# Kernel optimization log

Hardware: AMD Instinct MI355X
Metric: run time of the kernel (lower is better)

The kernel has to match this reference:

```python
import jax, jax.numpy as jnp
import numpy as np

B, IN_DIM, HID, OUT_DIM, K = 16384, 400, 24, 4096, 64


def setup_inputs() -> dict:
    key = jax.random.key(0)
    ks = jax.random.split(key, 20)
    bnd = 1.0 / np.sqrt(IN_DIM)

    def factorized_eps(k, shape):
        # sign(x)*sqrt(|x|) of small gaussian noise, outer-product factorized
        if len(shape) == 2:
            ko, ki = jax.random.split(k)
            eo = jax.random.normal(ko, (shape[0],)) * 0.001
            ei = jax.random.normal(ki, (shape[1],)) * 0.001
            f = lambda v: jnp.sign(v) * jnp.sqrt(jnp.abs(v))
            return jnp.outer(f(eo), f(ei))
        e = jax.random.normal(k, shape) * 0.001
        return jnp.sign(e) * jnp.sqrt(jnp.abs(e))

    sig2 = 0.5 / np.sqrt(HID)
    sig3 = 0.5 / np.sqrt(OUT_DIM)
    bnd24 = 1.0 / np.sqrt(HID)
    return {
        "x": jax.random.normal(ks[0], (B, IN_DIM), dtype=jnp.float32),
        "possible_moves": jax.random.randint(ks[1], (B, K), 0, OUT_DIM),
        "W1": jax.random.uniform(ks[2], (HID, IN_DIM), minval=-bnd, maxval=bnd),
        "b1": jax.random.uniform(ks[3], (HID,), minval=-bnd, maxval=bnd),
        "mu_w2": jax.random.uniform(ks[4], (HID, HID), minval=-bnd24, maxval=bnd24),
        "mu_b2": jax.random.uniform(ks[5], (HID,), minval=-bnd24, maxval=bnd24),
        "sigma_w2": jnp.full((HID, HID), sig2, dtype=jnp.float32),
        "sigma_b2": jnp.full((HID,), sig2, dtype=jnp.float32),
        "eps_w2": factorized_eps(ks[6], (HID, HID)),
        "eps_b2": factorized_eps(ks[7], (HID,)),
        "mu_w3": jax.random.uniform(ks[8], (OUT_DIM, HID), minval=-bnd24, maxval=bnd24),
        "mu_b3": jax.random.uniform(ks[9], (OUT_DIM,), minval=-bnd24, maxval=bnd24),
        "sigma_w3": jnp.full((OUT_DIM, HID), sig3, dtype=jnp.float32),
        "sigma_b3": jnp.full((OUT_DIM,), sig3, dtype=jnp.float32),
        "eps_w3": factorized_eps(ks[10], (OUT_DIM, HID)),
        "eps_b3": factorized_eps(ks[11], (OUT_DIM,)),
    }


def reference(x, possible_moves, W1, b1, mu_w2, mu_b2, sigma_w2, sigma_b2,
              eps_w2, eps_b2, mu_w3, mu_b3, sigma_w3, sigma_b3, eps_w3, eps_b3):
    h = jax.nn.relu(x @ W1.T + b1)
    w2 = mu_w2 + sigma_w2 * eps_w2
    h = jax.nn.relu(h @ w2.T + (mu_b2 + sigma_b2 * eps_b2))
    w3 = mu_w3 + sigma_w3 * eps_w3
    logits = h @ w3.T + (mu_b3 + sigma_b3 * eps_b3)  # [B, OUT_DIM]
    # scatter 1.0 at legal-move indices per row (vectorized LegalSoftmax)
    rows = jnp.arange(logits.shape[0])[:, None]
    mask = jnp.zeros(logits.shape, logits.dtype).at[rows, possible_moves].set(1.0)
    filtered = logits * mask
    return jnp.where(filtered == 0, -jnp.inf, filtered)
```

## Files before the change

### kernel.cpp

```cpp
#include <hip/hip_runtime.h>
#include <math.h>

#define BATCH 16384
#define IN_DIM 400
#define HID 24
#define OUT_DIM 4096
#define KMOV 64

#define SENT_BITS 0xFF7F0000u

__global__ __launch_bounds__(256) void precompute_w3(
    const float* __restrict__ mu_w3, const float* __restrict__ sigma_w3,
    const float* __restrict__ eps_w3, const float* __restrict__ mu_b3,
    const float* __restrict__ sigma_b3, const float* __restrict__ eps_b3,
    float* __restrict__ w3eff, float* __restrict__ b3eff) {
    const int stride = gridDim.x * blockDim.x;
    for (int i = blockIdx.x * blockDim.x + threadIdx.x; i < OUT_DIM * HID; i += stride)
        w3eff[i] = mu_w3[i] + sigma_w3[i] * eps_w3[i];
    for (int i = blockIdx.x * blockDim.x + threadIdx.x; i < OUT_DIM; i += stride)
        b3eff[i] = mu_b3[i] + sigma_b3[i] * eps_b3[i];
}

template <bool PRE>
__global__ __launch_bounds__(256) void noisy_fused(
    const float* __restrict__ x, const int* __restrict__ moves,
    const float* __restrict__ W1, const float* __restrict__ b1,
    const float* __restrict__ mu_w2, const float* __restrict__ mu_b2,
    const float* __restrict__ sigma_w2, const float* __restrict__ sigma_b2,
    const float* __restrict__ eps_w2, const float* __restrict__ eps_b2,
    const float* __restrict__ mu_w3, const float* __restrict__ mu_b3,
    const float* __restrict__ sigma_w3, const float* __restrict__ sigma_b3,
    const float* __restrict__ eps_w3, const float* __restrict__ eps_b3,
    const float* __restrict__ w3eff, const float* __restrict__ b3eff,
    float* __restrict__ out) {
    __shared__ float xs[IN_DIM];
    __shared__ float w2s[HID * HID];
    __shared__ float b2s[HID];
    __shared__ float h1s[HID];
    __shared__ float h2s[HID];

    const int tid = threadIdx.x;
    const int row = blockIdx.x;

    const float* xrow = x + (size_t)row * IN_DIM;
    for (int i = tid; i < IN_DIM; i += 256) xs[i] = xrow[i];
    for (int i = tid; i < HID * HID; i += 256)
        w2s[i] = mu_w2[i] + sigma_w2[i] * eps_w2[i];
    if (tid < HID) b2s[tid] = mu_b2[tid] + sigma_b2[tid] * eps_b2[tid];
    __syncthreads();

    if (tid < HID * 8) {
        const int u = tid >> 3, s = tid & 7;
        const float* w = W1 + u * IN_DIM + s * 50;
        const float* xp = xs + s * 50;
        float acc = 0.f;
#pragma unroll
        for (int k = 0; k < 50; ++k) acc += xp[k] * w[k];
        acc += __shfl_down(acc, 4, 8);
        acc += __shfl_down(acc, 2, 8);
        acc += __shfl_down(acc, 1, 8);
        if (s == 0) h1s[u] = fmaxf(acc + b1[u], 0.f);
    }
    __syncthreads();

    if (tid < HID) {
        float acc = b2s[tid];
#pragma unroll
        for (int j = 0; j < HID; ++j) acc += h1s[j] * w2s[tid * HID + j];
        h2s[tid] = fmaxf(acc, 0.f);
    }
    __syncthreads();

    const float SENT = __uint_as_float(SENT_BITS);
    float val = SENT;
    int idx = 0;
    if (tid < KMOV) {
        idx = moves[(size_t)row * KMOV + tid];
        float acc;
        if (PRE) {
            acc = b3eff[idx];
            const float4* wr = (const float4*)(w3eff + idx * HID);
#pragma unroll
            for (int q = 0; q < 6; ++q) {
                float4 w4 = wr[q];
                acc += h2s[q * 4 + 0] * w4.x + h2s[q * 4 + 1] * w4.y +
                       h2s[q * 4 + 2] * w4.z + h2s[q * 4 + 3] * w4.w;
            }
        } else {
            acc = mu_b3[idx] + sigma_b3[idx] * eps_b3[idx];
            const float4* mr = (const float4*)(mu_w3 + idx * HID);
            const float4* sr = (const float4*)(sigma_w3 + idx * HID);
            const float4* er = (const float4*)(eps_w3 + idx * HID);
#pragma unroll
            for (int q = 0; q < 6; ++q) {
                float4 m4 = mr[q], s4 = sr[q], e4 = er[q];
                acc += h2s[q * 4 + 0] * (m4.x + s4.x * e4.x) +
                       h2s[q * 4 + 1] * (m4.y + s4.y * e4.y) +
                       h2s[q * 4 + 2] * (m4.z + s4.z * e4.z) +
                       h2s[q * 4 + 3] * (m4.w + s4.w * e4.w);
            }
        }
        if (acc != 0.f) val = acc;
    }

    const float4 n4 = make_float4(SENT, SENT, SENT, SENT);
    float4* orow = (float4*)(out + (size_t)row * OUT_DIM);
#pragma unroll
    for (int i = 0; i < 4; ++i) orow[i * 256 + tid] = n4;
    __syncthreads();

    if (tid < KMOV) out[(size_t)row * OUT_DIM + idx] = val;
}

extern "C" void kernel_launch(void* const* d_in, const int* in_sizes, int n_in,
                              void* d_out, int out_size, void* d_ws, size_t ws_size,
                              hipStream_t stream) {
    const float* x        = (const float*)d_in[0];
    const int*   moves    = (const int*)d_in[1];
    const float* W1       = (const float*)d_in[2];
    const float* b1       = (const float*)d_in[3];
    const float* mu_w2    = (const float*)d_in[4];
    const float* mu_b2    = (const float*)d_in[5];
    const float* sigma_w2 = (const float*)d_in[6];
    const float* sigma_b2 = (const float*)d_in[7];
    const float* eps_w2   = (const float*)d_in[8];
    const float* eps_b2   = (const float*)d_in[9];
    const float* mu_w3    = (const float*)d_in[10];
    const float* mu_b3    = (const float*)d_in[11];
    const float* sigma_w3 = (const float*)d_in[12];
    const float* sigma_b3 = (const float*)d_in[13];
    const float* eps_w3   = (const float*)d_in[14];
    const float* eps_b3   = (const float*)d_in[15];
    float* out = (float*)d_out;

    float* w3eff = (float*)d_ws;
    float* b3eff = w3eff + OUT_DIM * HID;
    const size_t need = (size_t)(OUT_DIM * HID + OUT_DIM) * sizeof(float);

    if (ws_size >= need) {
        precompute_w3<<<256, 256, 0, stream>>>(mu_w3, sigma_w3, eps_w3,
                                               mu_b3, sigma_b3, eps_b3,
                                               w3eff, b3eff);
        noisy_fused<true><<<BATCH, 256, 0, stream>>>(
            x, moves, W1, b1, mu_w2, mu_b2, sigma_w2, sigma_b2, eps_w2, eps_b2,
            mu_w3, mu_b3, sigma_w3, sigma_b3, eps_w3, eps_b3, w3eff, b3eff, out);
    } else {
        noisy_fused<false><<<BATCH, 256, 0, stream>>>(
            x, moves, W1, b1, mu_w2, mu_b2, sigma_w2, sigma_b2, eps_w2, eps_b2,
            mu_w3, mu_b3, sigma_w3, sigma_b3, eps_w3, eps_b3, nullptr, nullptr, out);
    }
}
```

Measured before the change: 395.2 us.

## Issue sentinel fill early and restructure layer-1 dot products per wave

The sentinel fill of each output row and the load of the legal-move indices now happen at kernel start, so those stores overlap the MLP compute. The final barrier is removed; the barriers between layers already order the fill before the scatter. Layer 1 is rewritten so each of the four waves keeps a slice of x in registers and computes six hidden units. W1 rows are read coalesced across lanes and reduced with a full-wave xor shuffle, replacing the shared-memory x copy and the stride-50 per-thread reads. This uses every thread and improves memory coalescing, at the cost of more shuffle reductions and a few more registers.

```diff
diff --git a/kernel.cpp b/kernel.cpp
--- a/kernel.cpp
+++ b/kernel.cpp
@@ -33,33 +33,52 @@
     const float* __restrict__ eps_w3, const float* __restrict__ eps_b3,
     const float* __restrict__ w3eff, const float* __restrict__ b3eff,
     float* __restrict__ out) {
-    __shared__ float xs[IN_DIM];
     __shared__ float w2s[HID * HID];
     __shared__ float b2s[HID];
     __shared__ float h1s[HID];
     __shared__ float h2s[HID];
 
     const int tid = threadIdx.x;
+    const int lane = tid & 63;
+    const int wave = tid >> 6;
     const int row = blockIdx.x;
+    const float SENT = __uint_as_float(SENT_BITS);
 
-    const float* xrow = x + (size_t)row * IN_DIM;
-    for (int i = tid; i < IN_DIM; i += 256) xs[i] = xrow[i];
+    const float4 n4 = make_float4(SENT, SENT, SENT, SENT);
+    float4* orow = (float4*)(out + (size_t)row * OUT_DIM);
+#pragma unroll
+    for (int i = 0; i < 4; ++i) orow[i * 256 + tid] = n4;
+
+    int idx = 0;
+    if (tid < KMOV) idx = moves[(size_t)row * KMOV + tid];
+
     for (int i = tid; i < HID * HID; i += 256)
         w2s[i] = mu_w2[i] + sigma_w2[i] * eps_w2[i];
     if (tid < HID) b2s[tid] = mu_b2[tid] + sigma_b2[tid] * eps_b2[tid];
-    __syncthreads();
 
-    if (tid < HID * 8) {
-        const int u = tid >> 3, s = tid & 7;
-        const float* w = W1 + u * IN_DIM + s * 50;
-        const float* xp = xs + s * 50;
-        float acc = 0.f;
+    {
+        const float* xrow = x + (size_t)row * IN_DIM;
+        float xr[7];
 #pragma unroll
-        for (int k = 0; k < 50; ++k) acc += xp[k] * w[k];
-        acc += __shfl_down(acc, 4, 8);
-        acc += __shfl_down(acc, 2, 8);
-        acc += __shfl_down(acc, 1, 8);
-        if (s == 0) h1s[u] = fmaxf(acc + b1[u], 0.f);
+        for (int j = 0; j < 6; ++j) xr[j] = xrow[lane + 64 * j];
+        xr[6] = (lane < 16) ? xrow[lane + 384] : 0.f;
+
+#pragma unroll
+        for (int t = 0; t < 6; ++t) {
+            const int u = wave * 6 + t;
+            const float* wrow = W1 + u * IN_DIM;
+            float acc = 0.f;
+#pragma unroll
+            for (int j = 0; j < 6; ++j) acc += xr[j] * wrow[lane + 64 * j];
+            if (lane < 16) acc += xr[6] * wrow[lane + 384];
+            acc += __shfl_xor(acc, 32);
+            acc += __shfl_xor(acc, 16);
+            acc += __shfl_xor(acc, 8);
+            acc += __shfl_xor(acc, 4);
+            acc += __shfl_xor(acc, 2);
+            acc += __shfl_xor(acc, 1);
+            if (lane == 0) h1s[u] = fmaxf(acc + b1[u], 0.f);
+        }
     }
     __syncthreads();
 
@@ -71,11 +90,8 @@
     }
     __syncthreads();
 
-    const float SENT = __uint_as_float(SENT_BITS);
     float val = SENT;
-    int idx = 0;
     if (tid < KMOV) {
-        idx = moves[(size_t)row * KMOV + tid];
         float acc;
         if (PRE) {
             acc = b3eff[idx];
@@ -101,15 +117,9 @@
             }
         }
         if (acc != 0.f) val = acc;
+
+        out[(size_t)row * OUT_DIM + idx] = val;
     }
-
-    const float4 n4 = make_float4(SENT, SENT, SENT, SENT);
-    float4* orow = (float4*)(out + (size_t)row * OUT_DIM);
-#pragma unroll
-    for (int i = 0; i < 4; ++i) orow[i * 256 + tid] = n4;
-    __syncthreads();
-
-    if (tid < KMOV) out[(size_t)row * OUT_DIM + idx] = val;
 }
 
 extern "C" void kernel_launch(void* const* d_in, const int* in_sizes, int n_in,
```

After: 436.4 us. +10.4%, slower.
